# Optimization experiments

Hardware: AMD Instinct MI355X
Metric: run time of the kernel (lower is better)

## Reference

```python
import jax, jax.numpy as jnp
import numpy as np

N, E, D, L = 20000, 320000, 300, 5
V, EDIM, G, NC = 119, 7, 128, 6
BN_EPS = 1e-5


def _bn(z, g, b):
    # BatchNorm1d training-mode math: biased batch stats over the node axis
    mean = jnp.mean(z, axis=0)
    var = jnp.var(z, axis=0)
    return (z - mean) * jax.lax.rsqrt(var + BN_EPS) * g + b


def setup_inputs() -> dict:
    key = jax.random.key(0)
    ks = jax.random.split(key, 24)
    s = 0.05
    inp = {
        "x": jax.random.randint(ks[0], (N,), 0, V, dtype=jnp.int32),
        "edge_index": jax.random.randint(ks[1], (2, E), 0, N, dtype=jnp.int32),
        "edge_attr": jax.random.normal(ks[2], (E, EDIM), dtype=jnp.float32),
        "batch": jnp.sort(jax.random.randint(ks[3], (N,), 0, G, dtype=jnp.int32)),
        "node_emb": jax.random.normal(ks[4], (V, D), dtype=jnp.float32) * s,
        "edge_W": jax.random.normal(ks[5], (EDIM, D), dtype=jnp.float32) * s,
        "edge_b": jnp.zeros((D,), jnp.float32),
        "eps": jnp.zeros((L,), jnp.float32),  # train_eps=True, init 0
        "W1": jax.random.normal(ks[6], (L, D, D), dtype=jnp.float32) * s,
        "b1": jnp.zeros((L, D), jnp.float32),
        "g1": jnp.ones((L, D), jnp.float32),
        "be1": jnp.zeros((L, D), jnp.float32),
        "W2": jax.random.normal(ks[7], (L, D, D), dtype=jnp.float32) * s,
        "b2": jnp.zeros((L, D), jnp.float32),
        "g2": jnp.ones((L, D), jnp.float32),
        "be2": jnp.zeros((L, D), jnp.float32),
        "Wc1": jax.random.normal(ks[8], (D, D // 2), dtype=jnp.float32) * s,
        "bc1": jnp.zeros((D // 2,), jnp.float32),
        "Wc2": jax.random.normal(ks[9], (D // 2, NC), dtype=jnp.float32) * s,
        "bc2": jnp.zeros((NC,), jnp.float32),
    }
    return inp


def reference(x, edge_index, batch, edge_attr, node_emb, edge_W, edge_b, eps,
              W1, b1, g1, be1, W2, b2, g2, be2, Wc1, bc1, Wc2, bc2):
    src, dst = edge_index[0], edge_index[1]  # messages flow src -> dst (PyG x_j = row 0)
    h = node_emb[x]                          # [N, D] node encoder
    ea = edge_attr @ edge_W + edge_b         # [E, D] edge encoder
    for i in range(L):
        # GINEConv: sum_j relu(x_j + e_ij), then (1+eps)*x_i + agg, then MLP
        m = jax.nn.relu(h[src] + ea)                       # [E, D] gather + fuse
        agg = jax.ops.segment_sum(m, dst, num_segments=N)  # [N, D] scatter-add
        z = (1.0 + eps[i]) * h + agg
        z = jax.nn.relu(_bn(z @ W1[i] + b1[i], g1[i], be1[i]))
        z = z @ W2[i] + b2[i]
        h = jax.nn.relu(_bn(z, g2[i], be2[i]))             # outer BN + ReLU (dropout p=0)
    # global mean pool over graphs
    ones = jnp.ones((N,), h.dtype)
    counts = jax.ops.segment_sum(ones, batch, num_segments=G)
    pooled = jax.ops.segment_sum(h, batch, num_segments=G) / jnp.maximum(counts, 1.0)[:, None]
    out = jax.nn.relu(pooled @ Wc1 + bc1) @ Wc2 + bc2      # [G, NC]
    return out
```

## Files before the change

### kernel.cpp

```cpp
#include <hip/hip_runtime.h>
#include <hip/hip_bf16.h>
#include <stdint.h>

#define N_NODES 20000
#define N_EDGES 320000
#define DIM 300
#define ADIM 320
#define ROWS_PAD 20480
#define N_LAYERS 5
#define EDIM 7
#define NGRAPH 128
#define NCLS 6
#define DHALF 150
#define BN_EPS 1e-5f
#define NBUCK 16
#define BUCK_W 1250

#define CDIV(a, b) (((a) + (b) - 1) / (b))

typedef short bf16x8 __attribute__((ext_vector_type(8)));
typedef float f32x4 __attribute__((ext_vector_type(4)));
typedef unsigned short ushort_t;

__device__ __forceinline__ float bf2f(ushort_t u) {
    union { float f; uint32_t i; } v; v.i = ((uint32_t)u) << 16; return v.f;
}
__device__ __forceinline__ ushort_t f2bf(float f) {
    union { float f; uint32_t i; } v; v.f = f;
    uint32_t x = v.i;
    x += 0x7FFFu + ((x >> 16) & 1u);
    return (ushort_t)(x >> 16);
}

__device__ __forceinline__ void gload_lds16(const void* g, void* l) {
    __builtin_amdgcn_global_load_lds(
        (const __attribute__((address_space(1))) uint32_t*)g,
        (__attribute__((address_space(3))) uint32_t*)l, 16, 0, 0);
}

__global__ void node_enc_kernel(const int* __restrict__ x,
                                const float* __restrict__ node_emb,
                                ushort_t* __restrict__ h_bf) {
    int idx = blockIdx.x * blockDim.x + threadIdx.x;
    if (idx >= N_NODES * 40) return;
    int n = idx / 40;
    int d0 = (idx - n * 40) * 8;
    const float* src = node_emb + (size_t)x[n] * DIM;
    union { ushort_t u[8]; uint4 v; } o;
#pragma unroll
    for (int j = 0; j < 8; ++j) {
        int d = d0 + j;
        o.u[j] = (d < DIM) ? f2bf(src[d]) : (ushort_t)0;
    }
    *(uint4*)(h_bf + (size_t)n * ADIM + d0) = o.v;
}

__global__ void wt_prep_kernel(const float* __restrict__ W1,
                               const float* __restrict__ W2,
                               ushort_t* __restrict__ Wt) {
    int idx = blockIdx.x * blockDim.x + threadIdx.x;
    if (idx >= 10 * ADIM * ADIM) return;
    int mat = idx / (ADIM * ADIM);
    int rem = idx - mat * ADIM * ADIM;
    int n = rem / ADIM;
    int k = rem - n * ADIM;
    const float* src = (mat < 5) ? (W1 + (size_t)mat * DIM * DIM)
                                 : (W2 + (size_t)(mat - 5) * DIM * DIM);
    float v = (k < DIM && n < DIM) ? src[(size_t)k * DIM + n] : 0.0f;
    Wt[(size_t)mat * ADIM * ADIM + (size_t)n * ADIM + k] = f2bf(v);
}

__global__ void deg16_kernel(const int* __restrict__ src,
                             const int* __restrict__ dst,
                             int* __restrict__ deg16) {
    int e = blockIdx.x * blockDim.x + threadIdx.x;
    if (e < N_EDGES) atomicAdd(&deg16[dst[e] * NBUCK + src[e] / BUCK_W], 1);
}

__global__ void nodedeg_kernel(const int* __restrict__ deg16,
                               int* __restrict__ nodedeg) {
    int i = blockIdx.x * blockDim.x + threadIdx.x;
    if (i >= N_NODES) return;
    int tot = 0;
#pragma unroll
    for (int b = 0; b < NBUCK; ++b) tot += deg16[i * NBUCK + b];
    nodedeg[i] = tot;
}

__global__ void scan_kernel(const int* __restrict__ nodedeg,
                            int* __restrict__ off) {
    __shared__ int sh[1024];
    int t = threadIdx.x;
    int base = t * 20;
    int local[20];
    int s = 0;
#pragma unroll
    for (int j = 0; j < 20; ++j) {
        int i = base + j;
        int v = (i < N_NODES) ? nodedeg[i] : 0;
        local[j] = v;
        s += v;
    }
    sh[t] = s;
    __syncthreads();
    for (int o = 1; o < 1024; o <<= 1) {
        int v = sh[t];
        int add = (t >= o) ? sh[t - o] : 0;
        __syncthreads();
        sh[t] = v + add;
        __syncthreads();
    }
    int run = (t > 0) ? sh[t - 1] : 0;
#pragma unroll
    for (int j = 0; j < 20; ++j) {
        int i = base + j;
        if (i < N_NODES) {
            off[i] = run;
            run += local[j];
        }
    }
    if (t == 1023) off[N_NODES] = sh[1023];
}

__global__ void cur16_kernel(const int* __restrict__ deg16,
                             const int* __restrict__ off,
                             int* __restrict__ cur16) {
    int i = blockIdx.x * blockDim.x + threadIdx.x;
    if (i >= N_NODES) return;
    int c = off[i];
#pragma unroll
    for (int b = 0; b < NBUCK; ++b) {
        cur16[i * NBUCK + b] = c;
        c += deg16[i * NBUCK + b];
    }
}

__global__ void scatter_kernel(const int* __restrict__ src,
                               const int* __restrict__ dst,
                               const float* __restrict__ edge_attr,
                               int* __restrict__ cur16,
                               int* __restrict__ perm_src,
                               float* __restrict__ pea) {
    int e = blockIdx.x * blockDim.x + threadIdx.x;
    if (e >= N_EDGES) return;
    int s = src[e];
    int d = dst[e];
    int p = atomicAdd(&cur16[d * NBUCK + s / BUCK_W], 1);
    perm_src[p] = s;
    const float* ar = edge_attr + (size_t)e * EDIM;
    float* pr = pea + (size_t)p * 8;
#pragma unroll
    for (int j = 0; j < EDIM; ++j) pr[j] = ar[j];
    pr[7] = 0.0f;
}

#define MSG_BLOCKS 5000
template <bool BNH>
__global__ __launch_bounds__(256) void msg_kernel(
    const ushort_t* __restrict__ hsrc, ushort_t* __restrict__ z_bf,
    const int* __restrict__ off, const int* __restrict__ perm_src,
    const float* __restrict__ pea,
    const float* __restrict__ edge_W, const float* __restrict__ edge_b,
    const float* __restrict__ eps, int layer,
    const float* __restrict__ bs1, const float* __restrict__ bs2,
    const float* __restrict__ bg, const float* __restrict__ bbe) {
    int n = __builtin_amdgcn_readfirstlane(
        (int)((blockIdx.x * 256 + threadIdx.x) >> 6));
    if (n >= N_NODES) return;
    int lane = threadIdx.x & 63;

    float ew[5][7], eb[5], sc[5], sh[5];
#pragma unroll
    for (int c = 0; c < 5; ++c) {
        int d = c * 64 + lane;
        bool ok = (d < DIM);
        eb[c] = ok ? edge_b[d] : 0.0f;
#pragma unroll
        for (int j = 0; j < EDIM; ++j)
            ew[c][j] = ok ? edge_W[j * DIM + d] : 0.0f;
        if (BNH) {
            float s = 0.f, t = 0.f;
            if (ok) {
                const float invn = 1.0f / (float)N_NODES;
                float mean = bs1[d] * invn;
                float var = bs2[d] * invn - mean * mean;
                s = bg[d] * rsqrtf(var + BN_EPS);
                t = bbe[d] - mean * s;
            }
            sc[c] = s;
            sh[c] = t;
        }
    }
    float epsv = 1.0f + eps[layer];

    int p0 = __builtin_amdgcn_readfirstlane(off[n]);
    int p1 = __builtin_amdgcn_readfirstlane(off[n + 1]);
    float acc[5] = {0.f, 0.f, 0.f, 0.f, 0.f};
    float na0, na1, na2, na3, na4, na5, na6;
    float nhv[5];
    int s2i = 0;
    if (p0 < p1) {
        int s1i = __builtin_amdgcn_readfirstlane(perm_src[p0]);
        const float* ap = pea + (size_t)p0 * 8;
        na0 = ap[0]; na1 = ap[1]; na2 = ap[2]; na3 = ap[3];
        na4 = ap[4]; na5 = ap[5]; na6 = ap[6];
        const ushort_t* hr = hsrc + (size_t)s1i * ADIM;
#pragma unroll
        for (int c = 0; c < 5; ++c) nhv[c] = bf2f(hr[c * 64 + lane]);
        if (p0 + 1 < p1) s2i = __builtin_amdgcn_readfirstlane(perm_src[p0 + 1]);
    }
    for (int p = p0; p < p1; ++p) {
        float ca0 = na0, ca1 = na1, ca2 = na2, ca3 = na3;
        float ca4 = na4, ca5 = na5, ca6 = na6;
        float chv[5];
#pragma unroll
        for (int c = 0; c < 5; ++c) chv[c] = nhv[c];
        if (p + 1 < p1) {
            const float* ap = pea + (size_t)(p + 1) * 8;
            na0 = ap[0]; na1 = ap[1]; na2 = ap[2]; na3 = ap[3];
            na4 = ap[4]; na5 = ap[5]; na6 = ap[6];
            const ushort_t* hr = hsrc + (size_t)s2i * ADIM;
#pragma unroll
            for (int c = 0; c < 5; ++c) nhv[c] = bf2f(hr[c * 64 + lane]);
            if (p + 2 < p1)
                s2i = __builtin_amdgcn_readfirstlane(perm_src[p + 2]);
        }
#pragma unroll
        for (int c = 0; c < 5; ++c) {
            float hv = BNH ? fmaxf(chv[c] * sc[c] + sh[c], 0.0f) : chv[c];
            float ea = eb[c];
            ea += ca0 * ew[c][0];
            ea += ca1 * ew[c][1];
            ea += ca2 * ew[c][2];
            ea += ca3 * ew[c][3];
            ea += ca4 * ew[c][4];
            ea += ca5 * ew[c][5];
            ea += ca6 * ew[c][6];
            acc[c] += fmaxf(hv + ea, 0.0f);
        }
    }
    const ushort_t* hn = hsrc + (size_t)n * ADIM;
    ushort_t* zr = z_bf + (size_t)n * ADIM;
#pragma unroll
    for (int c = 0; c < 5; ++c) {
        int d = c * 64 + lane;
        float hv = bf2f(hn[d]);
        if (BNH) hv = fmaxf(hv * sc[c] + sh[c], 0.0f);
        zr[d] = f2bf(epsv * hv + acc[c]);
    }
}

__device__ __forceinline__ int swz(int row, int k8) {
    return ((row << 7) + (k8 << 4)) ^ ((row & 7) << 4);
}

template <bool BNA>
__global__ __launch_bounds__(256) void gemm_kernel(
    const ushort_t* __restrict__ A, const ushort_t* __restrict__ Wt,
    ushort_t* __restrict__ Ybf,
    const float* __restrict__ in_s1, const float* __restrict__ in_s2,
    const float* __restrict__ bn_g, const float* __restrict__ bn_be,
    float* __restrict__ gs1, float* __restrict__ gs2) {
    __shared__ ushort_t sA[128 * 64];
    __shared__ ushort_t sB[80 * 64];
    __shared__ float sRed[4 * 160];
    __shared__ float s_scale[ADIM], s_shift[ADIM];
    char* sAc = (char*)sA;
    char* sBc = (char*)sB;

    int tid = threadIdx.x;
    int lane = tid & 63;
    int wv = tid >> 6;
    int wgid = blockIdx.x;
    int xcd = wgid & 7, slot = wgid >> 3;
    int rb = xcd * 20 + (slot >> 2);
    int ct = slot & 3;
    int row0 = rb * 128;
    int col0 = ct * 80;
    int l15 = lane & 15, l4 = lane >> 4;
    int lr = lane >> 3;
    int k8 = lane & 7;
    int k8x = k8 ^ lr;

    if (BNA) {
        for (int d = tid; d < ADIM; d += 256) {
            float sc = 0.f, sh = 0.f;
            if (d < DIM) {
                const float invn = 1.0f / (float)N_NODES;
                float mean = in_s1[d] * invn;
                float var = in_s2[d] * invn - mean * mean;
                sc = bn_g[d] * rsqrtf(var + BN_EPS);
                sh = bn_be[d] - mean * sc;
            }
            s_scale[d] = sc;
            s_shift[d] = sh;
        }
        __syncthreads();
    }

    f32x4 acc[2][5];
#pragma unroll
    for (int m = 0; m < 2; ++m)
#pragma unroll
        for (int n = 0; n < 5; ++n) acc[m][n] = (f32x4){0.f, 0.f, 0.f, 0.f};

    for (int kt = 0; kt < 5; ++kt) {
        int k0 = kt * 64;
        if (!BNA) {
#pragma unroll
            for (int it = 0; it < 4; ++it) {
                int c = wv * 4 + it;
                int row = c * 8 + lr;
                const ushort_t* g = A + (size_t)(row0 + row) * ADIM + k0 + k8x * 8;
                gload_lds16(g, sAc + c * 1024);
            }
        } else {
#pragma unroll
            for (int it = 0; it < 4; ++it) {
                int idx = tid + it * 256;
                int row = idx >> 3, kc = idx & 7;
                const ushort_t* g = A + (size_t)(row0 + row) * ADIM + k0 + kc * 8;
                union { ushort_t u[8]; uint4 v; } in, o;
                in.v = *(const uint4*)g;
                int kb = k0 + kc * 8;
#pragma unroll
                for (int j = 0; j < 8; ++j)
                    o.u[j] = f2bf(fmaxf(bf2f(in.u[j]) * s_scale[kb + j] +
                                        s_shift[kb + j], 0.0f));
                *(uint4*)(sAc + swz(row, kc)) = o.v;
            }
        }
        for (int c = wv; c < 10; c += 4) {
            int row = c * 8 + lr;
            const ushort_t* g = Wt + (size_t)(col0 + row) * ADIM + k0 + k8x * 8;
            gload_lds16(g, sBc + c * 1024);
        }
        __syncthreads();

#pragma unroll
        for (int kk = 0; kk < 2; ++kk) {
            bf16x8 a[2], b[5];
#pragma unroll
            for (int m = 0; m < 2; ++m)
                a[m] = *(const bf16x8*)(sAc + swz(wv * 32 + m * 16 + l15, kk * 4 + l4));
#pragma unroll
            for (int n = 0; n < 5; ++n)
                b[n] = *(const bf16x8*)(sBc + swz(n * 16 + l15, kk * 4 + l4));
#pragma unroll
            for (int m = 0; m < 2; ++m)
#pragma unroll
                for (int n = 0; n < 5; ++n)
                    acc[m][n] = __builtin_amdgcn_mfma_f32_16x16x32_bf16(
                        a[m], b[n], acc[m][n], 0, 0, 0);
        }
        __syncthreads();
    }

#pragma unroll
    for (int n = 0; n < 5; ++n) {
        int col = col0 + n * 16 + l15;
        float s1 = 0.f, s2 = 0.f;
#pragma unroll
        for (int m = 0; m < 2; ++m) {
#pragma unroll
            for (int r = 0; r < 4; ++r) {
                int row = row0 + wv * 32 + m * 16 + l4 * 4 + r;
                float v = acc[m][n][r];
                if (row < N_NODES && col < DIM) {
                    Ybf[(size_t)row * ADIM + col] = f2bf(v);
                    s1 += v;
                    s2 += v * v;
                }
            }
        }
        s1 += __shfl_xor(s1, 16, 64);
        s1 += __shfl_xor(s1, 32, 64);
        s2 += __shfl_xor(s2, 16, 64);
        s2 += __shfl_xor(s2, 32, 64);
        if (l4 == 0) {
            sRed[wv * 160 + n * 16 + l15] = s1;
            sRed[wv * 160 + 80 + n * 16 + l15] = s2;
        }
    }
    __syncthreads();
    if (tid < 160) {
        float v = sRed[tid] + sRed[160 + tid] + sRed[320 + tid] + sRed[480 + tid];
        int cc = (tid < 80) ? tid : tid - 80;
        int col = col0 + cc;
        if (col < DIM) atomicAdd(((tid < 80) ? gs1 : gs2) + col, v);
    }
}

__device__ __forceinline__ int lbound(const int* __restrict__ batch, int g) {
    int lo = 0, hi = N_NODES;
    while (lo < hi) {
        int mid = (lo + hi) >> 1;
        if (batch[mid] < g) lo = mid + 1; else hi = mid;
    }
    return lo;
}

__global__ void pool_kernel(const ushort_t* __restrict__ y_bf,
                            const int* __restrict__ batch,
                            float* __restrict__ pooled,
                            float* __restrict__ counts,
                            const float* __restrict__ bs1,
                            const float* __restrict__ bs2,
                            const float* __restrict__ bg,
                            const float* __restrict__ bbe) {
    int g = blockIdx.x;
    int chunk = blockIdx.y;
    int d = threadIdx.x;
    int s = lbound(batch, g);
    int e = lbound(batch, g + 1);
    if (chunk == 0 && d == 0) counts[g] = (float)(e - s);
    if (d >= DIM) return;
    const float invn = 1.0f / (float)N_NODES;
    float mean = bs1[d] * invn;
    float var = bs2[d] * invn - mean * mean;
    float sc = bg[d] * rsqrtf(var + BN_EPS);
    float sh = bbe[d] - mean * sc;
    int len = e - s;
    int per = (len + 3) >> 2;
    int r0 = s + chunk * per;
    int r1 = min(r0 + per, e);
    float a = 0.f;
    for (int r = r0; r < r1; ++r)
        a += fmaxf(bf2f(y_bf[(size_t)r * ADIM + d]) * sc + sh, 0.0f);
    if (r1 > r0) atomicAdd(&pooled[(size_t)g * DIM + d], a);
}

__global__ void mlp1_kernel(const float* __restrict__ pooled,
                            const float* __restrict__ counts,
                            const float* __restrict__ Wc1,
                            const float* __restrict__ bc1,
                            float* __restrict__ hidden) {
    int g = blockIdx.x;
    int j = threadIdx.x;
    if (j >= DHALF) return;
    float inv = 1.0f / fmaxf(counts[g], 1.0f);
    const float* prow = pooled + (size_t)g * DIM;
    float acc = 0.0f;
    for (int k = 0; k < DIM; ++k) acc += prow[k] * Wc1[k * DHALF + j];
    hidden[g * DHALF + j] = fmaxf(acc * inv + bc1[j], 0.0f);
}

__global__ void mlp2_kernel(const float* __restrict__ hidden,
                            const float* __restrict__ Wc2,
                            const float* __restrict__ bc2,
                            float* __restrict__ out) {
    int idx = blockIdx.x * blockDim.x + threadIdx.x;
    if (idx >= NGRAPH * NCLS) return;
    int g = idx / NCLS;
    int c = idx - g * NCLS;
    const float* hrow = hidden + g * DHALF;
    float acc = bc2[c];
    for (int j = 0; j < DHALF; ++j) acc += hrow[j] * Wc2[j * NCLS + c];
    out[idx] = acc;
}

extern "C" void kernel_launch(void* const* d_in, const int* in_sizes, int n_in,
                              void* d_out, int out_size, void* d_ws, size_t ws_size,
                              hipStream_t stream) {
    const int*   x         = (const int*)d_in[0];
    const int*   edge_index= (const int*)d_in[1];
    const float* edge_attr = (const float*)d_in[2];
    const int*   batch     = (const int*)d_in[3];
    const float* node_emb  = (const float*)d_in[4];
    const float* edge_W    = (const float*)d_in[5];
    const float* edge_b    = (const float*)d_in[6];
    const float* eps       = (const float*)d_in[7];
    const float* W1        = (const float*)d_in[8];
    const float* g1        = (const float*)d_in[10];
    const float* be1       = (const float*)d_in[11];
    const float* W2        = (const float*)d_in[12];
    const float* g2        = (const float*)d_in[14];
    const float* be2       = (const float*)d_in[15];
    const float* Wc1       = (const float*)d_in[16];
    const float* bc1       = (const float*)d_in[17];
    const float* Wc2       = (const float*)d_in[18];
    const float* bc2       = (const float*)d_in[19];
    float* out = (float*)d_out;

    const int* src = edge_index;
    const int* dst = edge_index + N_EDGES;

    char* w = (char*)d_ws;
    size_t cur_off = 0;
    auto alloc = [&](size_t bytes) {
        char* p = w + cur_off;
        cur_off += (bytes + 63) & ~(size_t)63;
        return p;
    };
    const size_t AROW = (size_t)ROWS_PAD * ADIM;
    ushort_t* h_bf  = (ushort_t*)alloc(AROW * 2);
    ushort_t* zab   = (ushort_t*)alloc(AROW * 2);
    ushort_t* y1bf  = (ushort_t*)alloc(AROW * 2);
    ushort_t* y2bf  = (ushort_t*)alloc(AROW * 2);
    ushort_t* Wt    = (ushort_t*)alloc((size_t)10 * ADIM * ADIM * 2);
    int*      deg16 = (int*)alloc((size_t)N_NODES * NBUCK * 4);
    int*      cur16 = (int*)alloc((size_t)N_NODES * NBUCK * 4);
    int*      nodedeg = (int*)alloc((size_t)N_NODES * 4);
    int*      off   = (int*)alloc((N_NODES + 1) * 4);
    int*      psrc  = (int*)alloc((size_t)N_EDGES * 4);
    float*    pea   = (float*)alloc((size_t)N_EDGES * 8 * 4);
    float*    sbuf  = (float*)alloc((size_t)N_LAYERS * 4 * ADIM * 4);
    float*    pooled= (float*)alloc((size_t)NGRAPH * DIM * 4);
    float*    counts= (float*)alloc(NGRAPH * 4);
    float*    hidden= (float*)alloc((size_t)NGRAPH * DHALF * 4);

    auto sa1 = [&](int i) { return sbuf + ((size_t)i * 4 + 0) * ADIM; };
    auto sa2 = [&](int i) { return sbuf + ((size_t)i * 4 + 1) * ADIM; };
    auto sb1 = [&](int i) { return sbuf + ((size_t)i * 4 + 2) * ADIM; };
    auto sb2 = [&](int i) { return sbuf + ((size_t)i * 4 + 3) * ADIM; };

    hipMemsetAsync(deg16, 0, (size_t)N_NODES * NBUCK * 4, stream);
    hipMemsetAsync(zab + (size_t)N_NODES * ADIM, 0,
                   (size_t)(ROWS_PAD - N_NODES) * ADIM * 2, stream);
    hipMemsetAsync(sbuf, 0, (size_t)N_LAYERS * 4 * ADIM * 4, stream);

    node_enc_kernel<<<CDIV(N_NODES * 40, 256), 256, 0, stream>>>(x, node_emb, h_bf);
    wt_prep_kernel<<<CDIV(10 * ADIM * ADIM, 256), 256, 0, stream>>>(W1, W2, Wt);
    deg16_kernel<<<CDIV(N_EDGES, 256), 256, 0, stream>>>(src, dst, deg16);
    nodedeg_kernel<<<CDIV(N_NODES, 256), 256, 0, stream>>>(deg16, nodedeg);
    scan_kernel<<<1, 1024, 0, stream>>>(nodedeg, off);
    cur16_kernel<<<CDIV(N_NODES, 256), 256, 0, stream>>>(deg16, off, cur16);
    scatter_kernel<<<CDIV(N_EDGES, 256), 256, 0, stream>>>(src, dst, edge_attr,
                                                           cur16, psrc, pea);

    const int GEMM_BLOCKS = (ROWS_PAD / 128) * 4;

    for (int i = 0; i < N_LAYERS; ++i) {
        if (i == 0)
            msg_kernel<false><<<MSG_BLOCKS, 256, 0, stream>>>(
                h_bf, zab, off, psrc, pea, edge_W, edge_b, eps, i,
                nullptr, nullptr, nullptr, nullptr);
        else
            msg_kernel<true><<<MSG_BLOCKS, 256, 0, stream>>>(
                y2bf, zab, off, psrc, pea, edge_W, edge_b, eps, i,
                sb1(i - 1), sb2(i - 1), g2 + (i - 1) * DIM, be2 + (i - 1) * DIM);
        gemm_kernel<false><<<GEMM_BLOCKS, 256, 0, stream>>>(
            zab, Wt + (size_t)i * ADIM * ADIM, y1bf,
            nullptr, nullptr, nullptr, nullptr, sa1(i), sa2(i));
        gemm_kernel<true><<<GEMM_BLOCKS, 256, 0, stream>>>(
            y1bf, Wt + (size_t)(5 + i) * ADIM * ADIM, y2bf,
            sa1(i), sa2(i), g1 + i * DIM, be1 + i * DIM, sb1(i), sb2(i));
    }

    hipMemsetAsync(pooled, 0, (size_t)NGRAPH * DIM * 4, stream);
    dim3 pgrid(NGRAPH, 4);
    pool_kernel<<<pgrid, ADIM, 0, stream>>>(y2bf, batch, pooled, counts,
                                            sb1(N_LAYERS - 1), sb2(N_LAYERS - 1),
                                            g2 + (N_LAYERS - 1) * DIM,
                                            be2 + (N_LAYERS - 1) * DIM);
    mlp1_kernel<<<NGRAPH, 192, 0, stream>>>(pooled, counts, Wc1, bc1, hidden);
    mlp2_kernel<<<CDIV(NGRAPH * NCLS, 256), 256, 0, stream>>>(hidden, Wc2, bc2, out);
}
```

Measured before the change: 586.0 us.

## Store node features in lane-interleaved layout so message gathers use dword loads

```diff
diff --git a/kernel.cpp b/kernel.cpp
--- a/kernel.cpp
+++ b/kernel.cpp
@@ -6,6 +6,7 @@
 #define N_EDGES 320000
 #define DIM 300
 #define ADIM 320
+#define PR 384
 #define ROWS_PAD 20480
 #define N_LAYERS 5
 #define EDIM 7
@@ -25,6 +26,12 @@
 __device__ __forceinline__ float bf2f(ushort_t u) {
     union { float f; uint32_t i; } v; v.i = ((uint32_t)u) << 16; return v.f;
 }
+__device__ __forceinline__ float lo16(uint32_t w) {
+    union { float f; uint32_t i; } v; v.i = w << 16; return v.f;
+}
+__device__ __forceinline__ float hi16(uint32_t w) {
+    union { float f; uint32_t i; } v; v.i = w & 0xffff0000u; return v.f;
+}
 __device__ __forceinline__ ushort_t f2bf(float f) {
     union { float f; uint32_t i; } v; v.f = f;
     uint32_t x = v.i;
@@ -40,19 +47,22 @@
 
 __global__ void node_enc_kernel(const int* __restrict__ x,
                                 const float* __restrict__ node_emb,
-                                ushort_t* __restrict__ h_bf) {
+                                ushort_t* __restrict__ hperm) {
     int idx = blockIdx.x * blockDim.x + threadIdx.x;
-    if (idx >= N_NODES * 40) return;
-    int n = idx / 40;
-    int d0 = (idx - n * 40) * 8;
+    if (idx >= N_NODES * 64) return;
+    int n = idx >> 6, l = idx & 63;
     const float* src = node_emb + (size_t)x[n] * DIM;
-    union { ushort_t u[8]; uint4 v; } o;
-#pragma unroll
-    for (int j = 0; j < 8; ++j) {
-        int d = d0 + j;
-        o.u[j] = (d < DIM) ? f2bf(src[d]) : (ushort_t)0;
-    }
-    *(uint4*)(h_bf + (size_t)n * ADIM + d0) = o.v;
+    ushort_t u[6];
+#pragma unroll
+    for (int c = 0; c < 5; ++c) {
+        int d = c * 64 + l;
+        u[c] = (d < DIM) ? f2bf(src[d]) : (ushort_t)0;
+    }
+    u[5] = 0;
+    uint32_t* dst = (uint32_t*)(hperm + (size_t)n * PR + l * 6);
+    dst[0] = ((uint32_t)(unsigned short)u[1] << 16) | (unsigned short)u[0];
+    dst[1] = ((uint32_t)(unsigned short)u[3] << 16) | (unsigned short)u[2];
+    dst[2] = ((uint32_t)(unsigned short)u[5] << 16) | (unsigned short)u[4];
 }
 
 __global__ void wt_prep_kernel(const float* __restrict__ W1,
@@ -157,7 +167,7 @@
 #define MSG_BLOCKS 5000
 template <bool BNH>
 __global__ __launch_bounds__(256) void msg_kernel(
-    const ushort_t* __restrict__ hsrc, ushort_t* __restrict__ z_bf,
+    const ushort_t* __restrict__ hperm, ushort_t* __restrict__ z_bf,
     const int* __restrict__ off, const int* __restrict__ perm_src,
     const float* __restrict__ pea,
     const float* __restrict__ edge_W, const float* __restrict__ edge_b,
@@ -168,6 +178,8 @@
         (int)((blockIdx.x * 256 + threadIdx.x) >> 6));
     if (n >= N_NODES) return;
     int lane = threadIdx.x & 63;
+    bool ok4 = (lane < DIM - 256);
+    const int loff = lane * 6;
 
     float ew[5][7], eb[5], sc[5], sh[5];
 #pragma unroll
@@ -196,38 +208,37 @@
     int p0 = __builtin_amdgcn_readfirstlane(off[n]);
     int p1 = __builtin_amdgcn_readfirstlane(off[n + 1]);
     float acc[5] = {0.f, 0.f, 0.f, 0.f, 0.f};
+    uint32_t nw0, nw1, nw2;
     float na0, na1, na2, na3, na4, na5, na6;
-    float nhv[5];
     int s2i = 0;
     if (p0 < p1) {
         int s1i = __builtin_amdgcn_readfirstlane(perm_src[p0]);
         const float* ap = pea + (size_t)p0 * 8;
         na0 = ap[0]; na1 = ap[1]; na2 = ap[2]; na3 = ap[3];
         na4 = ap[4]; na5 = ap[5]; na6 = ap[6];
-        const ushort_t* hr = hsrc + (size_t)s1i * ADIM;
-#pragma unroll
-        for (int c = 0; c < 5; ++c) nhv[c] = bf2f(hr[c * 64 + lane]);
+        const uint32_t* hw = (const uint32_t*)(hperm + (size_t)s1i * PR + loff);
+        nw0 = hw[0]; nw1 = hw[1]; nw2 = hw[2];
         if (p0 + 1 < p1) s2i = __builtin_amdgcn_readfirstlane(perm_src[p0 + 1]);
     }
     for (int p = p0; p < p1; ++p) {
+        uint32_t cw0 = nw0, cw1 = nw1, cw2 = nw2;
         float ca0 = na0, ca1 = na1, ca2 = na2, ca3 = na3;
         float ca4 = na4, ca5 = na5, ca6 = na6;
-        float chv[5];
-#pragma unroll
-        for (int c = 0; c < 5; ++c) chv[c] = nhv[c];
         if (p + 1 < p1) {
             const float* ap = pea + (size_t)(p + 1) * 8;
             na0 = ap[0]; na1 = ap[1]; na2 = ap[2]; na3 = ap[3];
             na4 = ap[4]; na5 = ap[5]; na6 = ap[6];
-            const ushort_t* hr = hsrc + (size_t)s2i * ADIM;
-#pragma unroll
-            for (int c = 0; c < 5; ++c) nhv[c] = bf2f(hr[c * 64 + lane]);
+            const uint32_t* hw =
+                (const uint32_t*)(hperm + (size_t)s2i * PR + loff);
+            nw0 = hw[0]; nw1 = hw[1]; nw2 = hw[2];
             if (p + 2 < p1)
                 s2i = __builtin_amdgcn_readfirstlane(perm_src[p + 2]);
         }
+        float hv[5] = {lo16(cw0), hi16(cw0), lo16(cw1), hi16(cw1),
+                       ok4 ? lo16(cw2) : 0.0f};
 #pragma unroll
         for (int c = 0; c < 5; ++c) {
-            float hv = BNH ? fmaxf(chv[c] * sc[c] + sh[c], 0.0f) : chv[c];
+            float h = BNH ? fmaxf(hv[c] * sc[c] + sh[c], 0.0f) : hv[c];
             float ea = eb[c];
             ea += ca0 * ew[c][0];
             ea += ca1 * ew[c][1];
@@ -236,17 +247,21 @@
             ea += ca4 * ew[c][4];
             ea += ca5 * ew[c][5];
             ea += ca6 * ew[c][6];
-            acc[c] += fmaxf(hv + ea, 0.0f);
-        }
-    }
-    const ushort_t* hn = hsrc + (size_t)n * ADIM;
-    ushort_t* zr = z_bf + (size_t)n * ADIM;
-#pragma unroll
-    for (int c = 0; c < 5; ++c) {
-        int d = c * 64 + lane;
-        float hv = bf2f(hn[d]);
-        if (BNH) hv = fmaxf(hv * sc[c] + sh[c], 0.0f);
-        zr[d] = f2bf(epsv * hv + acc[c]);
+            acc[c] += fmaxf(h + ea, 0.0f);
+        }
+    }
+    {
+        const uint32_t* hw = (const uint32_t*)(hperm + (size_t)n * PR + loff);
+        uint32_t w0 = hw[0], w1 = hw[1], w2 = hw[2];
+        float hv[5] = {lo16(w0), hi16(w0), lo16(w1), hi16(w1),
+                       ok4 ? lo16(w2) : 0.0f};
+        ushort_t* zr = z_bf + (size_t)n * ADIM;
+#pragma unroll
+        for (int c = 0; c < 5; ++c) {
+            float h = hv[c];
+            if (BNH) h = fmaxf(h * sc[c] + sh[c], 0.0f);
+            zr[c * 64 + lane] = f2bf(epsv * h + acc[c]);
+        }
     }
 }
 
@@ -254,7 +269,7 @@
     return ((row << 7) + (k8 << 4)) ^ ((row & 7) << 4);
 }
 
-template <bool BNA>
+template <bool BNA, bool OPERM>
 __global__ __launch_bounds__(256) void gemm_kernel(
     const ushort_t* __restrict__ A, const ushort_t* __restrict__ Wt,
     ushort_t* __restrict__ Ybf,
@@ -359,6 +374,7 @@
 #pragma unroll
     for (int n = 0; n < 5; ++n) {
         int col = col0 + n * 16 + l15;
+        size_t cofs = OPERM ? (size_t)((col & 63) * 6 + (col >> 6)) : (size_t)col;
         float s1 = 0.f, s2 = 0.f;
 #pragma unroll
         for (int m = 0; m < 2; ++m) {
@@ -367,7 +383,8 @@
                 int row = row0 + wv * 32 + m * 16 + l4 * 4 + r;
                 float v = acc[m][n][r];
                 if (row < N_NODES && col < DIM) {
-                    Ybf[(size_t)row * ADIM + col] = f2bf(v);
+                    if (OPERM) Ybf[(size_t)row * PR + cofs] = f2bf(v);
+                    else       Ybf[(size_t)row * ADIM + cofs] = f2bf(v);
                     s1 += v;
                     s2 += v * v;
                 }
@@ -400,7 +417,7 @@
     return lo;
 }
 
-__global__ void pool_kernel(const ushort_t* __restrict__ y_bf,
+__global__ void pool_kernel(const ushort_t* __restrict__ yperm,
                             const int* __restrict__ batch,
                             float* __restrict__ pooled,
                             float* __restrict__ counts,
@@ -420,13 +437,14 @@
     float var = bs2[d] * invn - mean * mean;
     float sc = bg[d] * rsqrtf(var + BN_EPS);
     float sh = bbe[d] - mean * sc;
+    int pofs = (d & 63) * 6 + (d >> 6);
     int len = e - s;
     int per = (len + 3) >> 2;
     int r0 = s + chunk * per;
     int r1 = min(r0 + per, e);
     float a = 0.f;
     for (int r = r0; r < r1; ++r)
-        a += fmaxf(bf2f(y_bf[(size_t)r * ADIM + d]) * sc + sh, 0.0f);
+        a += fmaxf(bf2f(yperm[(size_t)r * PR + pofs]) * sc + sh, 0.0f);
     if (r1 > r0) atomicAdd(&pooled[(size_t)g * DIM + d], a);
 }
 
@@ -493,10 +511,11 @@
         return p;
     };
     const size_t AROW = (size_t)ROWS_PAD * ADIM;
-    ushort_t* h_bf  = (ushort_t*)alloc(AROW * 2);
+    const size_t PROW = (size_t)N_NODES * PR;
+    ushort_t* hperm = (ushort_t*)alloc(PROW * 2);
+    ushort_t* y2pm  = (ushort_t*)alloc(PROW * 2);
     ushort_t* zab   = (ushort_t*)alloc(AROW * 2);
     ushort_t* y1bf  = (ushort_t*)alloc(AROW * 2);
-    ushort_t* y2bf  = (ushort_t*)alloc(AROW * 2);
     ushort_t* Wt    = (ushort_t*)alloc((size_t)10 * ADIM * ADIM * 2);
     int*      deg16 = (int*)alloc((size_t)N_NODES * NBUCK * 4);
     int*      cur16 = (int*)alloc((size_t)N_NODES * NBUCK * 4);
@@ -519,7 +538,7 @@
                    (size_t)(ROWS_PAD - N_NODES) * ADIM * 2, stream);
     hipMemsetAsync(sbuf, 0, (size_t)N_LAYERS * 4 * ADIM * 4, stream);
 
-    node_enc_kernel<<<CDIV(N_NODES * 40, 256), 256, 0, stream>>>(x, node_emb, h_bf);
+    node_enc_kernel<<<CDIV(N_NODES * 64, 256), 256, 0, stream>>>(x, node_emb, hperm);
     wt_prep_kernel<<<CDIV(10 * ADIM * ADIM, 256), 256, 0, stream>>>(W1, W2, Wt);
     deg16_kernel<<<CDIV(N_EDGES, 256), 256, 0, stream>>>(src, dst, deg16);
     nodedeg_kernel<<<CDIV(N_NODES, 256), 256, 0, stream>>>(deg16, nodedeg);
@@ -533,23 +552,23 @@
     for (int i = 0; i < N_LAYERS; ++i) {
         if (i == 0)
             msg_kernel<false><<<MSG_BLOCKS, 256, 0, stream>>>(
-                h_bf, zab, off, psrc, pea, edge_W, edge_b, eps, i,
+                hperm, zab, off, psrc, pea, edge_W, edge_b, eps, i,
                 nullptr, nullptr, nullptr, nullptr);
         else
             msg_kernel<true><<<MSG_BLOCKS, 256, 0, stream>>>(
-                y2bf, zab, off, psrc, pea, edge_W, edge_b, eps, i,
+                y2pm, zab, off, psrc, pea, edge_W, edge_b, eps, i,
                 sb1(i - 1), sb2(i - 1), g2 + (i - 1) * DIM, be2 + (i - 1) * DIM);
-        gemm_kernel<false><<<GEMM_BLOCKS, 256, 0, stream>>>(
+        gemm_kernel<false, false><<<GEMM_BLOCKS, 256, 0, stream>>>(
             zab, Wt + (size_t)i * ADIM * ADIM, y1bf,
             nullptr, nullptr, nullptr, nullptr, sa1(i), sa2(i));
-        gemm_kernel<true><<<GEMM_BLOCKS, 256, 0, stream>>>(
-            y1bf, Wt + (size_t)(5 + i) * ADIM * ADIM, y2bf,
+        gemm_kernel<true, true><<<GEMM_BLOCKS, 256, 0, stream>>>(
+            y1bf, Wt + (size_t)(5 + i) * ADIM * ADIM, y2pm,
             sa1(i), sa2(i), g1 + i * DIM, be1 + i * DIM, sb1(i), sb2(i));
     }
 
     hipMemsetAsync(pooled, 0, (size_t)NGRAPH * DIM * 4, stream);
     dim3 pgrid(NGRAPH, 4);
-    pool_kernel<<<pgrid, ADIM, 0, stream>>>(y2bf, batch, pooled, counts,
+    pool_kernel<<<pgrid, ADIM, 0, stream>>>(y2pm, batch, pooled, counts,
                                             sb1(N_LAYERS - 1), sb2(N_LAYERS - 1),
                                             g2 + (N_LAYERS - 1) * DIM,
                                             be2 + (N_LAYERS - 1) * DIM);
```

Result: no change. 586.8 us, median of 3 (+0.1%).
